# Optimization experiments

Hardware: AMD Instinct MI355X
Metric: run time of the kernel (lower is better)

## Reference

```python
import jax, jax.numpy as jnp
import numpy as np

# 8-neighborhood offsets (dy, dx) in the same order as the torch module,
# so bit i of the LBP code corresponds to offsets[i].
OFFSETS = ((-1, -1), (-1, 0), (-1, 1), (0, 1), (1, 1), (1, 0), (1, -1), (0, -1))
NUM_BINS = 256


def setup_inputs() -> dict:
    key = jax.random.key(0)
    x = jax.random.uniform(key, (64, 3, 512, 512), dtype=jnp.float32)
    return {"x": x}


def reference(x) -> jnp.ndarray:
    bs, _, H, W = x.shape
    # RGB -> grayscale, [bs, H, W]
    gray = 0.2989 * x[:, 0] + 0.587 * x[:, 1] + 0.114 * x[:, 2]
    # replicate-pad by 1 on each spatial side ('edge' == torch 'replicate')
    pad = jnp.pad(gray, ((0, 0), (1, 1), (1, 1)), mode="edge")

    # Accumulate the 8-bit LBP code directly (fuses the codes/weights pass).
    lbp = jnp.zeros((bs, H, W), dtype=jnp.int32)
    for i, (dy, dx) in enumerate(OFFSETS):
        neigh = pad[:, 1 + dy:1 + dy + H, 1 + dx:1 + dx + W]
        lbp = lbp + (neigh >= gray).astype(jnp.int32) * (1 << i)

    # 256-bin histogram per image via a single scatter-add (bincount-style),
    # replacing the O(256*H*W) looped equality sums of the original.
    batch_idx = jnp.arange(bs, dtype=jnp.int32)[:, None]          # [bs, 1]
    flat = lbp.reshape(bs, H * W)                                  # [bs, H*W]
    hist = jnp.zeros((bs, NUM_BINS), dtype=jnp.float32).at[batch_idx, flat].add(1.0)

    # L2-normalize each histogram.
    norm = jnp.sqrt(jnp.sum(hist * hist, axis=1, keepdims=True))
    return hist / (norm + 1e-6)
```

## Files before the change

### kernel.cpp

```cpp
#include <hip/hip_runtime.h>

#define IMG_H 512
#define IMG_W 512
#define PLANE (IMG_H * IMG_W)
#define NBATCH 64
#define NBINS 256
#define TSTRIP 16
#define WAVES_PER_BLOCK 4
#define STRIPS_PER_IMG (IMG_H / TSTRIP)
#define BLOCKS_PER_IMG (STRIPS_PER_IMG / WAVES_PER_BLOCK)
#define NBLOCKS (BLOCKS_PER_IMG * NBATCH)

#define GRAY(rr, gg, bb) (0.2989f * (rr) + 0.587f * (gg) + 0.114f * (bb))

__global__ __launch_bounds__(256) void lbp_strip_kernel(const float* __restrict__ x,
                                                        float* __restrict__ ws) {
    __shared__ unsigned int lh[NBINS];
    const int tid = threadIdx.x;
    lh[tid] = 0u;
    __syncthreads();

    const int lin = blockIdx.x;
    const int sid = (lin & 7) * (NBLOCKS / 8) + (lin >> 3);
    const int b   = sid >> 3;
    const int bg  = sid & 7;

    const int wav   = tid >> 6;
    const int lane  = tid & 63;
    const int strip = bg * WAVES_PER_BLOCK + wav;
    const int y0    = strip * TSTRIP;

    const float* rP = x + (size_t)b * 3 * PLANE;
    const float* gP = rP + PLANE;
    const float* bP = rP + 2 * PLANE;
    const int    cx = 8 * lane;

    float t_[10], m_[10], b_[10];

    #define LOADGRAY(arr, gy_)                                                     \
    do {                                                                           \
        int gy = (gy_);                                                            \
        gy = gy < 0 ? 0 : (gy > IMG_H - 1 ? IMG_H - 1 : gy);                       \
        size_t off = (size_t)gy * IMG_W + cx;                                      \
        float4 ra = *(const float4*)(rP + off), rb = *(const float4*)(rP + off + 4);\
        float4 ga = *(const float4*)(gP + off), gb = *(const float4*)(gP + off + 4);\
        float4 ba = *(const float4*)(bP + off), bb = *(const float4*)(bP + off + 4);\
        arr[1] = GRAY(ra.x, ga.x, ba.x); arr[2] = GRAY(ra.y, ga.y, ba.y);          \
        arr[3] = GRAY(ra.z, ga.z, ba.z); arr[4] = GRAY(ra.w, ga.w, ba.w);          \
        arr[5] = GRAY(rb.x, gb.x, bb.x); arr[6] = GRAY(rb.y, gb.y, bb.y);          \
        arr[7] = GRAY(rb.z, gb.z, bb.z); arr[8] = GRAY(rb.w, gb.w, bb.w);          \
        float lft = __shfl_up(arr[8], 1, 64);                                      \
        float rgt = __shfl_down(arr[1], 1, 64);                                    \
        arr[0] = (lane == 0)  ? arr[1] : lft;                                      \
        arr[9] = (lane == 63) ? arr[8] : rgt;                                      \
    } while (0)

    #define COMPUTE8()                                                             \
    do {                                                                           \
        _Pragma("unroll")                                                          \
        for (int p = 0; p < 8; ++p) {                                              \
            const float ctr = m_[p + 1];                                           \
            unsigned code = 0u;                                                    \
            code |= (t_[p    ] >= ctr) ? 1u   : 0u;                                \
            code |= (t_[p + 1] >= ctr) ? 2u   : 0u;                                \
            code |= (t_[p + 2] >= ctr) ? 4u   : 0u;                                \
            code |= (m_[p + 2] >= ctr) ? 8u   : 0u;                                \
            code |= (b_[p + 2] >= ctr) ? 16u  : 0u;                                \
            code |= (b_[p + 1] >= ctr) ? 32u  : 0u;                                \
            code |= (b_[p    ] >= ctr) ? 64u  : 0u;                                \
            code |= (m_[p    ] >= ctr) ? 128u : 0u;                                \
            atomicAdd(&lh[code], 1u);                                              \
        }                                                                          \
    } while (0)

    if ((strip & 1) == 0) {
        LOADGRAY(t_, y0 - 1);
        LOADGRAY(m_, y0);
        #pragma unroll 4
        for (int i = 0; i < TSTRIP; ++i) {
            LOADGRAY(b_, y0 + 1 + i);
            COMPUTE8();
            #pragma unroll
            for (int k = 0; k < 10; ++k) { t_[k] = m_[k]; m_[k] = b_[k]; }
        }
    } else {
        LOADGRAY(b_, y0 + TSTRIP);
        LOADGRAY(m_, y0 + TSTRIP - 1);
        #pragma unroll 4
        for (int i = 0; i < TSTRIP; ++i) {
            LOADGRAY(t_, y0 + TSTRIP - 2 - i);
            COMPUTE8();
            #pragma unroll
            for (int k = 0; k < 10; ++k) { b_[k] = m_[k]; m_[k] = t_[k]; }
        }
    }
    #undef LOADGRAY
    #undef COMPUTE8

    __syncthreads();
    ws[((size_t)b * BLOCKS_PER_IMG + bg) * NBINS + tid] = (float)lh[tid];
}

__global__ __launch_bounds__(256) void finalize_kernel(const float* __restrict__ ws,
                                                       float* __restrict__ out) {
    const int b = blockIdx.x;
    const int t = threadIdx.x;
    float s = 0.0f;
    #pragma unroll
    for (int k = 0; k < BLOCKS_PER_IMG; ++k)
        s += ws[((size_t)b * BLOCKS_PER_IMG + k) * NBINS + t];
    float ss = s * s;
    #pragma unroll
    for (int o = 32; o > 0; o >>= 1) ss += __shfl_down(ss, o, 64);
    __shared__ float wsum[4];
    if ((t & 63) == 0) wsum[t >> 6] = ss;
    __syncthreads();
    float tot = wsum[0] + wsum[1] + wsum[2] + wsum[3];
    out[b * NBINS + t] = s / (sqrtf(tot) + 1e-6f);
}

extern "C" void kernel_launch(void* const* d_in, const int* in_sizes, int n_in,
                              void* d_out, int out_size, void* d_ws, size_t ws_size,
                              hipStream_t stream) {
    const float* x = (const float*)d_in[0];
    float* out = (float*)d_out;
    float* ws  = (float*)d_ws;

    lbp_strip_kernel<<<NBLOCKS, 256, 0, stream>>>(x, ws);
    finalize_kernel<<<NBATCH, 256, 0, stream>>>(ws, out);
}
```

Before: 37.88 us.

## Share strip boundary gray rows between waves through LDS to cut halo reloads

Each wave now converts its first and last strip rows to grayscale once and stores them in a shared LDS row buffer. The block's outer halo rows are stored there too, so neighbouring waves read their halo rows from LDS instead of reloading and reconverting them from global memory. The old even/odd strip traversal direction is replaced by a single forward loop over the interior rows, followed by two final rows read from LDS. This removes the redundant halo global loads but adds a block barrier before compute and 20KB of LDS per block, which may lower occupancy.

```diff
diff --git a/kernel.cpp b/kernel.cpp
--- a/kernel.cpp
+++ b/kernel.cpp
@@ -6,54 +6,86 @@
 #define NBATCH 64
 #define NBINS 256
 #define TSTRIP 16
-#define WAVES_PER_BLOCK 4
-#define STRIPS_PER_IMG (IMG_H / TSTRIP)
-#define BLOCKS_PER_IMG (STRIPS_PER_IMG / WAVES_PER_BLOCK)
+#define WPB 4
+#define BLOCKS_PER_IMG 8
 #define NBLOCKS (BLOCKS_PER_IMG * NBATCH)
 
 #define GRAY(rr, gg, bb) (0.2989f * (rr) + 0.587f * (gg) + 0.114f * (bb))
 
 __global__ __launch_bounds__(256) void lbp_strip_kernel(const float* __restrict__ x,
                                                         float* __restrict__ ws) {
+    __shared__ float rowbuf[10][IMG_W];
     __shared__ unsigned int lh[NBINS];
+
     const int tid = threadIdx.x;
     lh[tid] = 0u;
-    __syncthreads();
 
     const int lin = blockIdx.x;
     const int sid = (lin & 7) * (NBLOCKS / 8) + (lin >> 3);
     const int b   = sid >> 3;
     const int bg  = sid & 7;
 
-    const int wav   = tid >> 6;
-    const int lane  = tid & 63;
-    const int strip = bg * WAVES_PER_BLOCK + wav;
-    const int y0    = strip * TSTRIP;
+    const int wav  = tid >> 6;
+    const int lane = tid & 63;
+    const int y0   = (bg * WPB + wav) * TSTRIP;
+    const int by0  = bg * (WPB * TSTRIP);
 
     const float* rP = x + (size_t)b * 3 * PLANE;
     const float* gP = rP + PLANE;
     const float* bP = rP + 2 * PLANE;
     const int    cx = 8 * lane;
 
-    float t_[10], m_[10], b_[10];
-
-    #define LOADGRAY(arr, gy_)                                                     \
-    do {                                                                           \
-        int gy = (gy_);                                                            \
-        gy = gy < 0 ? 0 : (gy > IMG_H - 1 ? IMG_H - 1 : gy);                       \
-        size_t off = (size_t)gy * IMG_W + cx;                                      \
+    #define GRAY8(gy_, o0, o1)                                                      \
+    do {                                                                            \
+        int gy = (gy_);                                                             \
+        gy = gy < 0 ? 0 : (gy > IMG_H - 1 ? IMG_H - 1 : gy);                        \
+        size_t off = (size_t)gy * IMG_W + cx;                                       \
         float4 ra = *(const float4*)(rP + off), rb = *(const float4*)(rP + off + 4);\
         float4 ga = *(const float4*)(gP + off), gb = *(const float4*)(gP + off + 4);\
         float4 ba = *(const float4*)(bP + off), bb = *(const float4*)(bP + off + 4);\
-        arr[1] = GRAY(ra.x, ga.x, ba.x); arr[2] = GRAY(ra.y, ga.y, ba.y);          \
-        arr[3] = GRAY(ra.z, ga.z, ba.z); arr[4] = GRAY(ra.w, ga.w, ba.w);          \
-        arr[5] = GRAY(rb.x, gb.x, bb.x); arr[6] = GRAY(rb.y, gb.y, bb.y);          \
-        arr[7] = GRAY(rb.z, gb.z, bb.z); arr[8] = GRAY(rb.w, gb.w, bb.w);          \
-        float lft = __shfl_up(arr[8], 1, 64);                                      \
-        float rgt = __shfl_down(arr[1], 1, 64);                                    \
-        arr[0] = (lane == 0)  ? arr[1] : lft;                                      \
-        arr[9] = (lane == 63) ? arr[8] : rgt;                                      \
+        o0.x = GRAY(ra.x, ga.x, ba.x); o0.y = GRAY(ra.y, ga.y, ba.y);               \
+        o0.z = GRAY(ra.z, ga.z, ba.z); o0.w = GRAY(ra.w, ga.w, ba.w);               \
+        o1.x = GRAY(rb.x, gb.x, bb.x); o1.y = GRAY(rb.y, gb.y, bb.y);               \
+        o1.z = GRAY(rb.z, gb.z, bb.z); o1.w = GRAY(rb.w, gb.w, bb.w);               \
     } while (0)
+
+    #define FILL(arr, o0, o1)                                                       \
+    do {                                                                            \
+        arr[1] = o0.x; arr[2] = o0.y; arr[3] = o0.z; arr[4] = o0.w;                 \
+        arr[5] = o1.x; arr[6] = o1.y; arr[7] = o1.z; arr[8] = o1.w;                 \
+        float lft = __shfl_up(arr[8], 1, 64);                                       \
+        float rgt = __shfl_down(arr[1], 1, 64);                                     \
+        arr[0] = (lane == 0)  ? arr[1] : lft;                                       \
+        arr[9] = (lane == 63) ? arr[8] : rgt;                                       \
+    } while (0)
+
+    #define LOADGRAY(arr, gy_)                                                      \
+    do { float4 _a, _b; GRAY8(gy_, _a, _b); FILL(arr, _a, _b); } while (0)
+
+    #define LOADLDS(arr, lr)                                                        \
+    do {                                                                            \
+        float4 _a = *(const float4*)&rowbuf[(lr)][cx];                              \
+        float4 _b = *(const float4*)&rowbuf[(lr)][cx + 4];                          \
+        FILL(arr, _a, _b);                                                          \
+    } while (0)
+
+    {
+        float4 a, c;
+        GRAY8(y0, a, c);
+        *(float4*)&rowbuf[2 * wav][cx] = a; *(float4*)&rowbuf[2 * wav][cx + 4] = c;
+        GRAY8(y0 + TSTRIP - 1, a, c);
+        *(float4*)&rowbuf[2 * wav + 1][cx] = a; *(float4*)&rowbuf[2 * wav + 1][cx + 4] = c;
+        if (wav == 0) {
+            GRAY8(by0 - 1, a, c);
+            *(float4*)&rowbuf[8][cx] = a; *(float4*)&rowbuf[8][cx + 4] = c;
+        } else if (wav == 3) {
+            GRAY8(by0 + WPB * TSTRIP, a, c);
+            *(float4*)&rowbuf[9][cx] = a; *(float4*)&rowbuf[9][cx + 4] = c;
+        }
+    }
+    __syncthreads();
+
+    float t_[10], m_[10], b_[10];
 
     #define COMPUTE8()                                                             \
     do {                                                                           \
@@ -73,29 +105,33 @@
         }                                                                          \
     } while (0)
 
-    if ((strip & 1) == 0) {
-        LOADGRAY(t_, y0 - 1);
-        LOADGRAY(m_, y0);
-        #pragma unroll 4
-        for (int i = 0; i < TSTRIP; ++i) {
-            LOADGRAY(b_, y0 + 1 + i);
-            COMPUTE8();
-            #pragma unroll
-            for (int k = 0; k < 10; ++k) { t_[k] = m_[k]; m_[k] = b_[k]; }
-        }
-    } else {
-        LOADGRAY(b_, y0 + TSTRIP);
-        LOADGRAY(m_, y0 + TSTRIP - 1);
-        #pragma unroll 4
-        for (int i = 0; i < TSTRIP; ++i) {
-            LOADGRAY(t_, y0 + TSTRIP - 2 - i);
-            COMPUTE8();
-            #pragma unroll
-            for (int k = 0; k < 10; ++k) { b_[k] = m_[k]; m_[k] = t_[k]; }
-        }
+    #define SHIFT()                                                                \
+    do {                                                                           \
+        _Pragma("unroll")                                                          \
+        for (int k = 0; k < 10; ++k) { t_[k] = m_[k]; m_[k] = b_[k]; }             \
+    } while (0)
+
+    LOADLDS(t_, (wav == 0) ? 8 : 2 * (wav - 1) + 1);
+    LOADLDS(m_, 2 * wav);
+
+    #pragma unroll 7
+    for (int i = 0; i < TSTRIP - 2; ++i) {
+        LOADGRAY(b_, y0 + 1 + i);
+        COMPUTE8();
+        SHIFT();
     }
+    LOADLDS(b_, 2 * wav + 1);
+    COMPUTE8();
+    SHIFT();
+    LOADLDS(b_, (wav == 3) ? 9 : 2 * (wav + 1));
+    COMPUTE8();
+
+    #undef GRAY8
+    #undef FILL
     #undef LOADGRAY
+    #undef LOADLDS
     #undef COMPUTE8
+    #undef SHIFT
 
     __syncthreads();
     ws[((size_t)b * BLOCKS_PER_IMG + bg) * NBINS + tid] = (float)lh[tid];
```

New measurement: 39.75 us. +4.9%, slower.
